# Kernel optimization log

Hardware: AMD Instinct MI355X
Metric: run time of the kernel (lower is better)

The kernel has to match this reference:

```python
import jax, jax.numpy as jnp
import numpy as np

NUM_HEADS = 8
HEAD_DIM = 32  # in_channels // num_heads = 256 // 8


def setup_inputs() -> dict:
    key = jax.random.key(0)
    k1, k2, k3, k4 = jax.random.split(key, 4)
    B, C, H, W = 16, 256, 64, 64
    N = (H // 2) * (W // 2)  # 1024
    return {
        "x": jax.random.normal(k1, (B, C, H, W), dtype=jnp.float32),
        "w_qkv": jax.random.normal(k2, (3 * C, C), dtype=jnp.float32) * (1.0 / np.sqrt(C)),
        "b_qkv": jax.random.normal(k3, (3 * C,), dtype=jnp.float32) * 0.02,
        "pos_encoding": jax.random.normal(k4, (1, N, HEAD_DIM), dtype=jnp.float32) * 0.02,
    }


def reference(x, w_qkv, b_qkv, pos_encoding):
    B, C, H, W = x.shape
    Hp, Wp = H // 2, W // 2
    N = Hp * Wp
    # 1x1 conv: [B,C,H,W] -> [B,3C,H,W]
    y = jnp.einsum('bchw,oc->bohw', x, w_qkv) + b_qkv[None, :, None, None]
    # 2x2 max pool, stride 2
    y = y.reshape(B, 3 * C, Hp, 2, Wp, 2).max(axis=(3, 5))  # [B,3C,Hp,Wp]
    # split into q,k,v heads: channel order is (3, heads, head_dim)
    qkv = y.reshape(B, 3, NUM_HEADS, HEAD_DIM, N)
    qkv = qkv.transpose(1, 0, 2, 4, 3)  # [3,B,h,N,d]
    q, k, v = qkv[0], qkv[1], qkv[2]
    q = q + pos_encoding[:, None, :, :]  # broadcast over heads -> [B,h,N,d]
    scale = HEAD_DIM ** (-0.5)
    attn = jnp.einsum('bhnd,bhmd->bhnm', q, k) * scale
    attn = jax.nn.softmax(attn, axis=-1)
    out = jnp.einsum('bhnm,bhmd->bhnd', attn, v)  # [B,h,N,d]
    # transpose(2,3) then reshape -> [B, C, Hp, Wp]
    out = out.transpose(0, 1, 3, 2).reshape(B, C, Hp, Wp)
    return out
```

## Files before the change

### kernel.cpp

```cpp
#include <hip/hip_runtime.h>
#include <hip/hip_bf16.h>

typedef __bf16 bf16;
typedef bf16 bf16x8 __attribute__((ext_vector_type(8)));
typedef float f32x4 __attribute__((ext_vector_type(4)));
typedef float f32x16 __attribute__((ext_vector_type(16)));
typedef unsigned int u32;
typedef u32 u32x2 __attribute__((ext_vector_type(2)));
typedef u32 u32x4 __attribute__((ext_vector_type(4)));
typedef int i32x2 __attribute__((ext_vector_type(2)));


__device__ __forceinline__ u32 packbf2(float lo, float hi) {
    unsigned short a = __builtin_bit_cast(unsigned short, (bf16)lo);
    unsigned short b = __builtin_bit_cast(unsigned short, (bf16)hi);
    return (u32)a | ((u32)b << 16);
}

#if __has_builtin(__builtin_amdgcn_exp2f)
#define EXP2(x) __builtin_amdgcn_exp2f(x)
#else
#define EXP2(x) __expf((x)*0.69314718055994531f)
#endif

__device__ __forceinline__ i32x2 pl32swap(u32 a, u32 b) {
#if __has_builtin(__builtin_amdgcn_permlane32_swap)
    return __builtin_amdgcn_permlane32_swap((int)a, (int)b, false, false);
#else
    int lid = __builtin_amdgcn_mbcnt_hi(~0u, __builtin_amdgcn_mbcnt_lo(~0u, 0));
    u32 ax = (u32)__shfl_xor((int)a, 32);
    u32 bx = (u32)__shfl_xor((int)b, 32);
    i32x2 r;
    r.x = (int)(lid < 32 ? a : bx);
    r.y = (int)(lid < 32 ? ax : b);
    return r;
#endif
}

__device__ __forceinline__ f32x16 zero16() {
    f32x16 z;
#pragma unroll
    for (int i = 0; i < 16; ++i) z[i] = 0.f;
    return z;
}

__device__ __forceinline__ void gload_lds16(const bf16* gsrc, bf16* ldst) {
    __builtin_amdgcn_global_load_lds(
        (const __attribute__((address_space(1))) void*)gsrc,
        (__attribute__((address_space(3))) void*)ldst, 16, 0, 0);
}

#define MEMFENCE()                               \
    do {                                         \
        asm volatile("" ::: "memory");           \
        __builtin_amdgcn_sched_barrier(0);       \
    } while (0)

#define WAITV(N)                                                   \
    do {                                                           \
        asm volatile("s_waitcnt vmcnt(" #N ")" ::: "memory");      \
        __builtin_amdgcn_sched_barrier(0);                         \
    } while (0)

#define WAITLGKM()                                                 \
    do {                                                           \
        asm volatile("s_waitcnt lgkmcnt(0)" ::: "memory");         \
        __builtin_amdgcn_sched_barrier(0);                         \
    } while (0)

__global__ __launch_bounds__(256) void k_transpose_x(const float* __restrict__ x,
                                                     bf16* __restrict__ xt) {
    __shared__ __align__(16) bf16 tile[64][72];
    int b = blockIdx.z, cb = blockIdx.y, pb = blockIdx.x;
    int c0 = cb * 64, p0 = pb * 64;
    int t = threadIdx.x;
    int pr = (t & 15) * 4;
    int cr = t >> 4;
    const float* xp = x + ((size_t)(b * 256 + c0)) * 4096 + p0;
    for (int pass = 0; pass < 4; ++pass) {
        int c = cr + pass * 16;
        float4 v = *reinterpret_cast<const float4*>(xp + (size_t)c * 4096 + pr);
        tile[pr + 0][c] = (bf16)v.x;
        tile[pr + 1][c] = (bf16)v.y;
        tile[pr + 2][c] = (bf16)v.z;
        tile[pr + 3][c] = (bf16)v.w;
    }
    __syncthreads();
    bf16* op = xt + ((size_t)(b * 4096 + p0)) * 256 + c0;
    int c8 = (t & 7) * 8;
    int prow = t >> 3;
    for (int pass = 0; pass < 2; ++pass) {
        int p = prow + pass * 32;
        *reinterpret_cast<bf16x8*>(op + (size_t)p * 256 + c8) =
            *reinterpret_cast<const bf16x8*>(&tile[p][c8]);
    }
}

__global__ __launch_bounds__(256) void k_convert_w(const float* __restrict__ w,
                                                   bf16* __restrict__ wb) {
    int i = (blockIdx.x * 256 + threadIdx.x) * 8;
    float4 a = *reinterpret_cast<const float4*>(w + i);
    float4 b4 = *reinterpret_cast<const float4*>(w + i + 4);
    bf16x8 o;
    o[0] = (bf16)a.x;  o[1] = (bf16)a.y;  o[2] = (bf16)a.z;  o[3] = (bf16)a.w;
    o[4] = (bf16)b4.x; o[5] = (bf16)b4.y; o[6] = (bf16)b4.z; o[7] = (bf16)b4.w;
    *reinterpret_cast<bf16x8*>(wb + i) = o;
}

__global__ __launch_bounds__(256) void k_gemm_pool(const bf16* __restrict__ xt,
                                                   const bf16* __restrict__ wb,
                                                   const float* __restrict__ bias,
                                                   const float* __restrict__ pos,
                                                   bf16* __restrict__ Qb,
                                                   bf16* __restrict__ Kb,
                                                   bf16* __restrict__ Vb) {
    __shared__ __align__(16) bf16 bt[128 * 256];
    int b = blockIdx.y, nt = blockIdx.x;
    int p0 = nt * 128;
    int t = threadIdx.x;
    int w = t >> 6, lane = t & 63, g = lane >> 4, q = lane & 15;

    const bf16* xtp = xt + ((size_t)(b * 4096 + p0)) * 256;
    const bf16* wb_w = wb + (size_t)(w * 32) * 256;

    {
        int srow = t >> 5;
        int scb = t & 31;
        int wbase_row = w * 2;
#pragma unroll
        for (int pass = 0; pass < 16; ++pass) {
            int row = srow + pass * 8;
            int p = 2 * (row & 15) + ((row >> 4) & 1) + ((row >> 5) & 1) * 64 +
                    ((row >> 6) & 1) * 32;
            const bf16* gs = xtp + (size_t)p * 256 + ((scb ^ (row & 7)) << 3);
            gload_lds16(gs, bt + (pass * 8 + wbase_row) * 256);
        }
    }
    MEMFENCE();

    bf16x8 Ac[4], An[4];
#define LOADA(MT, KC, DST)                                                     \
    {                                                                          \
        _Pragma("unroll")                                                      \
        for (int ks = 0; ks < 2; ++ks)                                         \
            _Pragma("unroll")                                                  \
            for (int fr = 0; fr < 2; ++fr)                                     \
                DST[ks * 2 + fr] = *reinterpret_cast<const bf16x8*>(           \
                    wb_w + (size_t)((MT) * 128 + fr * 16 + q) * 256 +          \
                    (KC) * 64 + ks * 32 + g * 8);                              \
    }
    LOADA(0, 0, Ac);
    MEMFENCE();

    WAITV(4);
    __builtin_amdgcn_s_barrier();
    __builtin_amdgcn_sched_barrier(0);

    const float QSCALE = 0.2550406682649681f;

    for (int mt = 0; mt < 6; ++mt) {
        f32x4 acc[2][8];
#pragma unroll
        for (int fr = 0; fr < 2; ++fr)
#pragma unroll
            for (int fc = 0; fc < 8; ++fc) acc[fr][fc] = (f32x4){0.f, 0.f, 0.f, 0.f};

#pragma unroll
        for (int kc = 0; kc < 4; ++kc) {
            if (kc < 3) {
                LOADA(mt, kc + 1, An);
            } else if (mt < 5) {
                LOADA(mt + 1, 0, An);
            }
#pragma unroll
            for (int ks = 0; ks < 2; ++ks) {
#pragma unroll
                for (int fc = 0; fc < 8; ++fc) {
                    int co = kc * 64 + (((ks * 4 + g) ^ (q & 7)) << 3);
                    bf16x8 bfv = *reinterpret_cast<const bf16x8*>(
                        &bt[(fc * 16 + q) * 256 + co]);
                    acc[0][fc] = __builtin_amdgcn_mfma_f32_16x16x32_bf16(
                        Ac[ks * 2 + 0], bfv, acc[0][fc], 0, 0, 0);
                    acc[1][fc] = __builtin_amdgcn_mfma_f32_16x16x32_bf16(
                        Ac[ks * 2 + 1], bfv, acc[1][fc], 0, 0, 0);
                }
            }
#pragma unroll
            for (int i = 0; i < 4; ++i) Ac[i] = An[i];
        }

        int m0 = mt * 128;
        int sec = mt >> 1;
        int hh = ((m0 >> 5) + w) & 7;
        size_t bh = (size_t)(b * 8 + hh) * 32768;
#pragma unroll
        for (int fr = 0; fr < 2; ++fr) {
            int dbase = fr * 16 + g * 4;
            float4 bs = *reinterpret_cast<const float4*>(&bias[m0 + w * 32 + dbase]);
#pragma unroll
            for (int G = 0; G < 2; ++G) {
                int n_g = nt * 32 + G * 16 + q;
                float vm[4];
#pragma unroll
                for (int r = 0; r < 4; ++r) {
                    float a0 = fmaxf(acc[fr][4 * G + 0][r], acc[fr][4 * G + 1][r]);
                    float a1 = fmaxf(acc[fr][4 * G + 2][r], acc[fr][4 * G + 3][r]);
                    vm[r] = fmaxf(a0, a1) + ((const float*)&bs)[r];
                }
                if (sec == 0) {
                    float4 pv = *reinterpret_cast<const float4*>(
                        &pos[(size_t)n_g * 32 + dbase]);
                    u32x2 o2 = {packbf2((vm[0] + pv.x) * QSCALE, (vm[1] + pv.y) * QSCALE),
                                packbf2((vm[2] + pv.z) * QSCALE, (vm[3] + pv.w) * QSCALE)};
                    *reinterpret_cast<u32x2*>(Qb + bh + (size_t)n_g * 32 + dbase) = o2;
                } else if (sec == 1) {
                    u32x2 o2 = {packbf2(vm[0], vm[1]), packbf2(vm[2], vm[3])};
                    *reinterpret_cast<u32x2*>(Kb + bh + (size_t)n_g * 32 + dbase) = o2;
                } else {
#pragma unroll
                    for (int r = 0; r < 4; ++r)
                        Vb[bh + (size_t)(dbase + r) * 1024 + n_g] = (bf16)vm[r];
                }
            }
        }
    }
#undef LOADA
}

#define SUBTILE_FULL(K0, K1, V0, V1)                                           \
    {                                                                          \
        f32x16 s = __builtin_amdgcn_mfma_f32_32x32x16_bf16(K0, qf0, zero16(), 0, 0, 0); \
        s = __builtin_amdgcn_mfma_f32_32x32x16_bf16(K1, qf1, s, 0, 0, 0);      \
        float p[16];                                                           \
        _Pragma("unroll")                                                      \
        for (int r = 0; r < 16; ++r) p[r] = EXP2(s[r]);                        \
        float ts = (((p[0]+p[1])+(p[2]+p[3]))+((p[4]+p[5])+(p[6]+p[7]))) +     \
                   (((p[8]+p[9])+(p[10]+p[11]))+((p[12]+p[13])+(p[14]+p[15])));\
        run_s += ts;                                                           \
        u32 pk0 = packbf2(p[0],p[1]),   pk1 = packbf2(p[2],p[3]);              \
        u32 pk2 = packbf2(p[4],p[5]),   pk3 = packbf2(p[6],p[7]);              \
        u32 pk4 = packbf2(p[8],p[9]),   pk5 = packbf2(p[10],p[11]);            \
        u32 pk6 = packbf2(p[12],p[13]), pk7 = packbf2(p[14],p[15]);            \
        i32x2 r02 = pl32swap(pk0, pk2); i32x2 r13 = pl32swap(pk1, pk3);        \
        i32x2 r46 = pl32swap(pk4, pk6); i32x2 r57 = pl32swap(pk5, pk7);        \
        u32x4 b0v = {(u32)r02.x, (u32)r13.x, (u32)r02.y, (u32)r13.y};          \
        u32x4 b1v = {(u32)r46.x, (u32)r57.x, (u32)r46.y, (u32)r57.y};          \
        bf16x8 pb0 = __builtin_bit_cast(bf16x8, b0v);                          \
        bf16x8 pb1 = __builtin_bit_cast(bf16x8, b1v);                          \
        o = __builtin_amdgcn_mfma_f32_32x32x16_bf16(V0, pb0, o, 0, 0, 0);      \
        o = __builtin_amdgcn_mfma_f32_32x32x16_bf16(V1, pb1, o, 0, 0, 0);      \
    }

__global__ __launch_bounds__(256) void k_attn(const bf16* __restrict__ Q,
                                              const bf16* __restrict__ K,
                                              const bf16* __restrict__ V,
                                              float* __restrict__ out) {
    __shared__ __align__(16) bf16 kt[2][2048];
    __shared__ __align__(16) bf16 vt[2][2048];
    int h = blockIdx.x, b = blockIdx.y, qb = blockIdx.z;
    int t = threadIdx.x, w = t >> 6, lane = t & 63;
    int lq = lane & 31, hi = lane >> 5, hi8 = hi * 8;
    size_t bh = (size_t)b * 8 + h;
    const bf16* Qp = Q + bh * 32768;
    const bf16* Kp = K + bh * 32768;
    const bf16* Vp = V + bh * 32768;
    float* Op = out + ((size_t)(b * 256 + h * 32)) * 1024;
    int q0 = qb * 128 + w * 32;

    bf16x8 qf0 = *reinterpret_cast<const bf16x8*>(Qp + (size_t)(q0 + lq) * 32 + hi8);
    bf16x8 qf1 = *reinterpret_cast<const bf16x8*>(Qp + (size_t)(q0 + lq) * 32 + 16 + hi8);

    int srow = lane & 31;
    int sh = w & 1, isV = w >> 1;
    const bf16* sg0;
    if (!isV) sg0 = Kp + (size_t)(sh * 32 + srow) * 32 + (lane >> 5) * 8;
    else      sg0 = Vp + (size_t)srow * 1024 + sh * 32 + (lane >> 5) * 8;
    const bf16* sg1 = sg0 + 16;
    int d0 = sh * 1024, d1 = sh * 1024 + 512;

#define STAGE64(BB, TT)                                                        \
    do {                                                                       \
        if (!isV) {                                                            \
            gload_lds16(sg0 + (size_t)(TT) * 2048, &kt[BB][d0]);               \
            gload_lds16(sg1 + (size_t)(TT) * 2048, &kt[BB][d1]);               \
        } else {                                                               \
            gload_lds16(sg0 + (TT) * 64, &vt[BB][d0]);                         \
            gload_lds16(sg1 + (TT) * 64, &vt[BB][d1]);                         \
        }                                                                      \
    } while (0)

    f32x16 o = zero16();
    float run_s = 0.f;

    STAGE64(0, 0);
    MEMFENCE();
    STAGE64(1, 1);
    MEMFENCE();

    for (int tt = 0; tt < 16; ++tt) {
        int cur = tt & 1;
        if (tt < 15) { WAITV(2); } else { WAITV(0); }
        __builtin_amdgcn_s_barrier();
        __builtin_amdgcn_sched_barrier(0);

        bf16x8 ka0 = *reinterpret_cast<const bf16x8*>(&kt[cur][hi * 256 + lq * 8]);
        bf16x8 ka1 = *reinterpret_cast<const bf16x8*>(&kt[cur][512 + hi * 256 + lq * 8]);
        bf16x8 va0 = *reinterpret_cast<const bf16x8*>(&vt[cur][hi * 256 + lq * 8]);
        bf16x8 va1 = *reinterpret_cast<const bf16x8*>(&vt[cur][512 + hi * 256 + lq * 8]);
        bf16x8 kb0 = *reinterpret_cast<const bf16x8*>(&kt[cur][1024 + hi * 256 + lq * 8]);
        bf16x8 kb1 = *reinterpret_cast<const bf16x8*>(&kt[cur][1536 + hi * 256 + lq * 8]);
        bf16x8 vb0 = *reinterpret_cast<const bf16x8*>(&vt[cur][1024 + hi * 256 + lq * 8]);
        bf16x8 vb1 = *reinterpret_cast<const bf16x8*>(&vt[cur][1536 + hi * 256 + lq * 8]);
        WAITLGKM();
        __builtin_amdgcn_s_barrier();
        __builtin_amdgcn_sched_barrier(0);
        if (tt < 14) STAGE64(cur, tt + 2);
        MEMFENCE();

        SUBTILE_FULL(ka0, ka1, va0, va1);
        SUBTILE_FULL(kb0, kb1, vb0, vb1);
    }
#undef STAGE64

    i32x2 rs = pl32swap(__builtin_bit_cast(u32, run_s), __builtin_bit_cast(u32, run_s));
    float tot = __builtin_bit_cast(float, (u32)rs.x) + __builtin_bit_cast(float, (u32)rs.y);
    float inv = 1.0f / tot;

#pragma unroll
    for (int r = 0; r < 16; ++r) {
        int dd = (r & 3) + 8 * (r >> 2) + 4 * hi;
        Op[(size_t)dd * 1024 + q0 + lq] = o[r] * inv;
    }
}

extern "C" void kernel_launch(void* const* d_in, const int* in_sizes, int n_in,
                              void* d_out, int out_size, void* d_ws, size_t ws_size,
                              hipStream_t stream) {
    const float* x = (const float*)d_in[0];
    const float* w = (const float*)d_in[1];
    const float* bias = (const float*)d_in[2];
    const float* pos = (const float*)d_in[3];
    float* outp = (float*)d_out;

    char* ws = (char*)d_ws;
    bf16* xt = (bf16*)(ws);
    bf16* wb = (bf16*)(ws + 33554432);
    bf16* Qb = (bf16*)(ws + 33947648);
    bf16* Kb = (bf16*)(ws + 42336256);
    bf16* Vb = (bf16*)(ws + 50724864);

    k_transpose_x<<<dim3(64, 4, 16), 256, 0, stream>>>(x, xt);
    k_convert_w<<<dim3(96), 256, 0, stream>>>(w, wb);
    k_gemm_pool<<<dim3(32, 16), 256, 0, stream>>>(xt, wb, bias, pos, Qb, Kb, Vb);
    k_attn<<<dim3(8, 16, 8), 256, 0, stream>>>(Qb, Kb, Vb, outp);
}
```

Measured before the change: 97.88 us.

## Fuse x transpose and bf16 conversion into GEMM-pool LDS staging

Removes the separate transpose kernel and its 32MB bf16 intermediate. The GEMM kernel now reads fp32 x directly with float4 loads, converts to bf16 and scatters into swizzled, pool-ordered LDS rows. This drops one launch plus a full write and reread of x. The cost is scalar 2-byte LDS stores with possible bank conflicts, and losing the async global-to-LDS load overlap with the first A loads.

```diff
diff --git a/kernel.cpp b/kernel.cpp
--- a/kernel.cpp
+++ b/kernel.cpp
@@ -68,34 +68,6 @@
         __builtin_amdgcn_sched_barrier(0);                         \
     } while (0)
 
-__global__ __launch_bounds__(256) void k_transpose_x(const float* __restrict__ x,
-                                                     bf16* __restrict__ xt) {
-    __shared__ __align__(16) bf16 tile[64][72];
-    int b = blockIdx.z, cb = blockIdx.y, pb = blockIdx.x;
-    int c0 = cb * 64, p0 = pb * 64;
-    int t = threadIdx.x;
-    int pr = (t & 15) * 4;
-    int cr = t >> 4;
-    const float* xp = x + ((size_t)(b * 256 + c0)) * 4096 + p0;
-    for (int pass = 0; pass < 4; ++pass) {
-        int c = cr + pass * 16;
-        float4 v = *reinterpret_cast<const float4*>(xp + (size_t)c * 4096 + pr);
-        tile[pr + 0][c] = (bf16)v.x;
-        tile[pr + 1][c] = (bf16)v.y;
-        tile[pr + 2][c] = (bf16)v.z;
-        tile[pr + 3][c] = (bf16)v.w;
-    }
-    __syncthreads();
-    bf16* op = xt + ((size_t)(b * 4096 + p0)) * 256 + c0;
-    int c8 = (t & 7) * 8;
-    int prow = t >> 3;
-    for (int pass = 0; pass < 2; ++pass) {
-        int p = prow + pass * 32;
-        *reinterpret_cast<bf16x8*>(op + (size_t)p * 256 + c8) =
-            *reinterpret_cast<const bf16x8*>(&tile[p][c8]);
-    }
-}
-
 __global__ __launch_bounds__(256) void k_convert_w(const float* __restrict__ w,
                                                    bf16* __restrict__ wb) {
     int i = (blockIdx.x * 256 + threadIdx.x) * 8;
@@ -107,7 +79,7 @@
     *reinterpret_cast<bf16x8*>(wb + i) = o;
 }
 
-__global__ __launch_bounds__(256) void k_gemm_pool(const bf16* __restrict__ xt,
+__global__ __launch_bounds__(256) void k_gemm_pool(const float* __restrict__ x,
                                                    const bf16* __restrict__ wb,
                                                    const float* __restrict__ bias,
                                                    const float* __restrict__ pos,
@@ -116,27 +88,34 @@
                                                    bf16* __restrict__ Vb) {
     __shared__ __align__(16) bf16 bt[128 * 256];
     int b = blockIdx.y, nt = blockIdx.x;
-    int p0 = nt * 128;
     int t = threadIdx.x;
     int w = t >> 6, lane = t & 63, g = lane >> 4, q = lane & 15;
 
-    const bf16* xtp = xt + ((size_t)(b * 4096 + p0)) * 256;
+    const float* xp = x + (size_t)b * 256 * 4096 + nt * 128;
     const bf16* wb_w = wb + (size_t)(w * 32) * 256;
 
     {
-        int srow = t >> 5;
-        int scb = t & 31;
-        int wbase_row = w * 2;
-#pragma unroll
-        for (int pass = 0; pass < 16; ++pass) {
-            int row = srow + pass * 8;
-            int p = 2 * (row & 15) + ((row >> 4) & 1) + ((row >> 5) & 1) * 64 +
-                    ((row >> 6) & 1) * 32;
-            const bf16* gs = xtp + (size_t)p * 256 + ((scb ^ (row & 7)) << 3);
-            gload_lds16(gs, bt + (pass * 8 + wbase_row) * 256);
+        int j0 = (t & 31) * 4;
+        int cbase = t >> 5;
+        int sb[4], key[4];
+#pragma unroll
+        for (int i = 0; i < 4; ++i) {
+            int j = j0 + i;
+            int s = ((j & 31) >> 1) | ((j & 1) << 4) |
+                    (((j >> 5) & 1) << 6) | (((j >> 6) & 1) << 5);
+            sb[i] = s * 256;
+            key[i] = (s & 7) << 3;
         }
-    }
-    MEMFENCE();
+#pragma unroll
+        for (int pass = 0; pass < 32; ++pass) {
+            int c = cbase + pass * 8;
+            float4 v = *reinterpret_cast<const float4*>(xp + (size_t)c * 4096 + j0);
+            bt[sb[0] + (c ^ key[0])] = (bf16)v.x;
+            bt[sb[1] + (c ^ key[1])] = (bf16)v.y;
+            bt[sb[2] + (c ^ key[2])] = (bf16)v.z;
+            bt[sb[3] + (c ^ key[3])] = (bf16)v.w;
+        }
+    }
 
     bf16x8 Ac[4], An[4];
 #define LOADA(MT, KC, DST)                                                     \
@@ -152,7 +131,7 @@
     LOADA(0, 0, Ac);
     MEMFENCE();
 
-    WAITV(4);
+    WAITLGKM();
     __builtin_amdgcn_s_barrier();
     __builtin_amdgcn_sched_barrier(0);
 
@@ -343,14 +322,12 @@
     float* outp = (float*)d_out;
 
     char* ws = (char*)d_ws;
-    bf16* xt = (bf16*)(ws);
-    bf16* wb = (bf16*)(ws + 33554432);
-    bf16* Qb = (bf16*)(ws + 33947648);
-    bf16* Kb = (bf16*)(ws + 42336256);
-    bf16* Vb = (bf16*)(ws + 50724864);
-
-    k_transpose_x<<<dim3(64, 4, 16), 256, 0, stream>>>(x, xt);
+    bf16* wb = (bf16*)(ws);
+    bf16* Qb = (bf16*)(ws + 393216);
+    bf16* Kb = (bf16*)(ws + 8781824);
+    bf16* Vb = (bf16*)(ws + 17170432);
+
     k_convert_w<<<dim3(96), 256, 0, stream>>>(w, wb);
-    k_gemm_pool<<<dim3(32, 16), 256, 0, stream>>>(xt, wb, bias, pos, Qb, Kb, Vb);
+    k_gemm_pool<<<dim3(32, 16), 256, 0, stream>>>(x, wb, bias, pos, Qb, Kb, Vb);
     k_attn<<<dim3(8, 16, 8), 256, 0, stream>>>(Qb, Kb, Vb, outp);
 }
```

Result: faster. 90.36 us (-7.7%).
